# Performance work log

Measured on AMD Instinct MI355X. Metric: run time of the kernel, lower is better.

Reference implementation:

```python
import jax, jax.numpy as jnp
import numpy as np
from jax import lax

NUM_HEADS = 8
FOCUSING_FACTOR = 3.0
KERNEL_SIZE = 5


def setup_inputs() -> dict:
    key = jax.random.key(0)
    ks = jax.random.split(key, 9)
    B, C, H, W = 16, 256, 64, 64
    s = 0.02
    return {
        "x": jax.random.normal(ks[0], (B, C, H, W), dtype=jnp.float32),
        "Wq": jax.random.normal(ks[1], (C, C), dtype=jnp.float32) * s,
        "bq": jax.random.normal(ks[2], (C,), dtype=jnp.float32) * s,
        "Wkv": jax.random.normal(ks[3], (2 * C, C), dtype=jnp.float32) * s,
        "bkv": jax.random.normal(ks[4], (2 * C,), dtype=jnp.float32) * s,
        "Wproj": jax.random.normal(ks[5], (C, C), dtype=jnp.float32) * s,
        "bproj": jax.random.normal(ks[6], (C,), dtype=jnp.float32) * s,
        "dwc_w": jax.random.normal(ks[7], (C // NUM_HEADS, 1, KERNEL_SIZE, KERNEL_SIZE), dtype=jnp.float32) * s,
        "dwc_b": jax.random.normal(ks[8], (C // NUM_HEADS,), dtype=jnp.float32) * s,
        "scale_param": jnp.zeros((1, 1, C), dtype=jnp.float32),
    }


def reference(x, Wq, bq, Wkv, bkv, Wproj, bproj, dwc_w, dwc_b, scale_param):
    B, C, H, W = x.shape
    nh = NUM_HEADS
    hd = C // nh
    N = H * W
    num = int(round(N ** 0.5))  # feature map side, N is a perfect square

    xt = x.reshape(B, C, N).transpose(0, 2, 1)  # [B, N, C]
    q = xt @ Wq.T + bq
    kv = xt @ Wkv.T + bkv  # [B, N, 2C] -> (2, C) split on last dim
    k, v = kv[..., :C], kv[..., C:]
    # positional_encoding is freshly-initialized zeros in the original forward -> no-op

    scale = jax.nn.softplus(scale_param)  # [1, 1, C]
    q = (jax.nn.relu(q) + 1e-6) / scale
    k = (jax.nn.relu(k) + 1e-6) / scale
    q_norm = jnp.linalg.norm(q, axis=-1, keepdims=True)
    k_norm = jnp.linalg.norm(k, axis=-1, keepdims=True)
    q = q ** FOCUSING_FACTOR
    k = k ** FOCUSING_FACTOR
    q = q / jnp.linalg.norm(q, axis=-1, keepdims=True) * q_norm
    k = k / jnp.linalg.norm(k, axis=-1, keepdims=True) * k_norm

    def split_heads(t):  # [B, N, C] -> [B*nh, N, hd]
        return t.reshape(B, N, nh, hd).transpose(0, 2, 1, 3).reshape(B * nh, N, hd)

    q, k, v = split_heads(q), split_heads(k), split_heads(v)

    # linear attention (kv path; i*j*(c+d) > c*d*(i+j) for these shapes)
    z = 1.0 / (jnp.einsum('bic,bc->bi', q, k.sum(axis=1)) + 1e-6)  # [BH, N]
    kv_state = jnp.einsum('bjc,bjd->bcd', k, v)  # [BH, hd, hd]
    out = jnp.einsum('bic,bcd->bid', q, kv_state) * z[..., None]  # [BH, N, hd]

    # depthwise conv on v feature map
    fm = v.transpose(0, 2, 1).reshape(B * nh, hd, num, num)
    fm = lax.conv_general_dilated(
        fm, dwc_w, window_strides=(1, 1),
        padding=[(KERNEL_SIZE // 2, KERNEL_SIZE // 2)] * 2,
        dimension_numbers=('NCHW', 'OIHW', 'NCHW'),
        feature_group_count=hd,
    ) + dwc_b[None, :, None, None]
    fm = fm.reshape(B * nh, hd, N).transpose(0, 2, 1)  # [BH, N, hd]

    out = out + fm
    out = out.reshape(B, nh, N, hd).transpose(0, 2, 1, 3).reshape(B, N, C)
    out = out @ Wproj.T + bproj
    return out.transpose(0, 2, 1).reshape(B, C, H, W)
```

## Files before the change

kernel.cpp:

```cpp
#include <hip/hip_runtime.h>
#include <math.h>

#define NB 16
#define NC 256
#define NN 4096
#define HD 32
#define BHD 128
#define KSPLIT 32

typedef unsigned short bf16_t;
typedef __attribute__((ext_vector_type(4))) float floatx4;
typedef __attribute__((ext_vector_type(16))) float floatx16;
typedef __attribute__((ext_vector_type(8))) short shortx8;

__device__ __forceinline__ float bf2f(unsigned int u16) {
  return __uint_as_float(u16 << 16);
}
__device__ __forceinline__ bf16_t f2bf(float f) {
  unsigned int u = __float_as_uint(f);
  return (bf16_t)((u + 0x7FFFu + ((u >> 16) & 1u)) >> 16);
}
__device__ __forceinline__ void bf8_expand(uint4 u, float* f) {
  f[0] = bf2f(u.x & 0xffffu); f[1] = bf2f(u.x >> 16);
  f[2] = bf2f(u.y & 0xffffu); f[3] = bf2f(u.y >> 16);
  f[4] = bf2f(u.z & 0xffffu); f[5] = bf2f(u.z >> 16);
  f[6] = bf2f(u.w & 0xffffu); f[7] = bf2f(u.w >> 16);
}
__device__ __forceinline__ float softplusf(float x) {
  return fmaxf(x, 0.0f) + log1pf(expf(-fabsf(x)));
}

__device__ __forceinline__ void gl_lds16(const void* g, void* l) {
  __builtin_amdgcn_global_load_lds(
      (const __attribute__((address_space(1))) unsigned int*)g,
      (__attribute__((address_space(3))) unsigned int*)l, 16, 0, 0);
}

__global__ __launch_bounds__(256) void k_prepx(
    const float* __restrict__ x, bf16_t* __restrict__ xbf)
{
  __shared__ float T[64][68];
  const int tid = threadIdx.x;
  const int n0 = blockIdx.x * 64, c0 = blockIdx.y * 64, b = blockIdx.z;
  const float* xb = x + (size_t)b * NC * NN;
#pragma unroll
  for (int it = 0; it < 4; ++it) {
    int c = it * 16 + (tid >> 4);
    int n4 = (tid & 15) * 4;
    float4 v = *(const float4*)(xb + (size_t)(c0 + c) * NN + n0 + n4);
    T[c][n4 + 0] = v.x; T[c][n4 + 1] = v.y;
    T[c][n4 + 2] = v.z; T[c][n4 + 3] = v.w;
  }
  __syncthreads();
  bf16_t* ob = xbf + (size_t)b * NN * NC;
#pragma unroll
  for (int it = 0; it < 2; ++it) {
    int n = it * 32 + (tid >> 3);
    int ch = (tid & 7) * 8;
    unsigned short e[8];
#pragma unroll
    for (int j = 0; j < 8; ++j) e[j] = f2bf(T[ch + j][n]);
    uint4 u;
    u.x = e[0] | ((unsigned)e[1] << 16); u.y = e[2] | ((unsigned)e[3] << 16);
    u.z = e[4] | ((unsigned)e[5] << 16); u.w = e[6] | ((unsigned)e[7] << 16);
    *(uint4*)(ob + (size_t)(n0 + n) * NC + c0 + ch) = u;
  }
}

__global__ __launch_bounds__(256) void k_prepw(
    const float* __restrict__ Wq, const float* __restrict__ Wkv,
    const float* __restrict__ Wp, const float* __restrict__ bq,
    const float* __restrict__ bkv, const float* __restrict__ sp,
    bf16_t* __restrict__ Wqkvb, bf16_t* __restrict__ Wpb,
    float* __restrict__ bias768, float* __restrict__ rscale)
{
  const int blk = blockIdx.x;
  const int tid = threadIdx.x;
  if (blk < 768) {
    const float* src = (blk < 256) ? (Wq + (size_t)blk * NC)
                                   : (Wkv + (size_t)(blk - 256) * NC);
    Wqkvb[(size_t)blk * NC + tid] = f2bf(src[tid]);
  } else if (blk < 1024) {
    int j = blk - 768;
    Wpb[(size_t)j * NC + tid] = f2bf(Wp[(size_t)j * NC + tid]);
  } else if (blk == 1024) {
    for (int i = tid; i < 768; i += 256)
      bias768[i] = (i < 256) ? bq[i] : bkv[i - 256];
  } else {
    rscale[tid] = 1.0f / softplusf(sp[tid]);
  }
}

__global__ __launch_bounds__(256) void k_qkv_mfma(
    const bf16_t* __restrict__ xbf, const bf16_t* __restrict__ Wqkvb,
    const float* __restrict__ bias768, bf16_t* __restrict__ qkv)
{
  __shared__ bf16_t As[128 * 32];
  __shared__ bf16_t Bs[128 * 32];
  const int tid = threadIdx.x;
  const int lane = tid & 63;
  const int w = tid >> 6;
  const int b = blockIdx.z;
  const int m0 = blockIdx.x * 128;
  const int n0 = blockIdx.y * 128;
  const bf16_t* Ab = xbf + ((size_t)b * NN + m0) * NC;
  const bf16_t* Bb = Wqkvb + (size_t)n0 * NC;

  const int wm = (w & 1) * 64;
  const int wn = (w >> 1) * 64;
  const int srow = w * 32 + (lane >> 2);
  const int scol = (((lane & 3) ^ ((lane >> 3) & 3))) * 8;
  const int fm = lane & 15;
  const int kg = lane >> 4;
  const int kga = kg ^ ((fm >> 1) & 3);

  floatx4 acc[4][4];
#pragma unroll
  for (int i = 0; i < 4; ++i)
#pragma unroll
    for (int j = 0; j < 4; ++j) {
      floatx4 z = {0.f, 0.f, 0.f, 0.f};
      acc[i][j] = z;
    }

  for (int k0 = 0; k0 < NC; k0 += 32) {
#pragma unroll
    for (int r = 0; r < 2; ++r) {
      gl_lds16(Ab + (size_t)(srow + r * 16) * NC + k0 + scol,
               &As[(w * 32 + r * 16) * 32]);
      gl_lds16(Bb + (size_t)(srow + r * 16) * NC + k0 + scol,
               &Bs[(w * 32 + r * 16) * 32]);
    }
    __syncthreads();
    shortx8 af[4], bfg[4];
#pragma unroll
    for (int t = 0; t < 4; ++t) {
      af[t]  = *(const shortx8*)&As[(wm + t * 16 + fm) * 32 + kga * 8];
      bfg[t] = *(const shortx8*)&Bs[(wn + t * 16 + fm) * 32 + kga * 8];
    }
#pragma unroll
    for (int tm = 0; tm < 4; ++tm)
#pragma unroll
      for (int tn = 0; tn < 4; ++tn)
        acc[tm][tn] = __builtin_amdgcn_mfma_f32_16x16x32_bf16(
            af[tm], bfg[tn], acc[tm][tn], 0, 0, 0);
    __syncthreads();
  }

  float bv[4];
#pragma unroll
  for (int tn = 0; tn < 4; ++tn)
    bv[tn] = bias768[n0 + wn + tn * 16 + fm];

  bf16_t* obase = qkv + ((size_t)b * NN + m0) * 768;
#pragma unroll
  for (int tm = 0; tm < 4; ++tm) {
    int mrow = wm + tm * 16 + kg * 4;
#pragma unroll
    for (int tn = 0; tn < 4; ++tn) {
      int n = n0 + wn + tn * 16 + fm;
#pragma unroll
      for (int r = 0; r < 4; ++r)
        obase[(size_t)(mrow + r) * 768 + n] = f2bf(acc[tm][tn][r] + bv[tn]);
    }
  }
}

__global__ __launch_bounds__(256) void k_focus(
    bf16_t* __restrict__ qkv, const float* __restrict__ rscale)
{
  const int lane = threadIdx.x & 63;
  const int w = threadIdx.x >> 6;
  const size_t t = (size_t)blockIdx.x * 4 + w;
  bf16_t* row = qkv + t * 768;
  ushort4 qu = *(ushort4*)(row + lane * 4);
  ushort4 ku = *(ushort4*)(row + 256 + lane * 4);
  float4 s4 = *(const float4*)(rscale + lane * 4);
  float q[4] = {bf2f(qu.x), bf2f(qu.y), bf2f(qu.z), bf2f(qu.w)};
  float k[4] = {bf2f(ku.x), bf2f(ku.y), bf2f(ku.z), bf2f(ku.w)};
  float rs[4] = {s4.x, s4.y, s4.z, s4.w};
  float q3[4], k3[4];
  float sq2 = 0.f, sq6 = 0.f, sk2 = 0.f, sk6 = 0.f;
#pragma unroll
  for (int i = 0; i < 4; ++i) {
    float qi = (fmaxf(q[i], 0.f) + 1e-6f) * rs[i];
    float ki = (fmaxf(k[i], 0.f) + 1e-6f) * rs[i];
    float qc = qi * qi * qi;
    float kc = ki * ki * ki;
    sq2 += qi * qi;  sk2 += ki * ki;
    sq6 += qc * qc;  sk6 += kc * kc;
    q3[i] = qc; k3[i] = kc;
  }
#pragma unroll
  for (int off = 32; off > 0; off >>= 1) {
    sq2 += __shfl_xor(sq2, off);
    sq6 += __shfl_xor(sq6, off);
    sk2 += __shfl_xor(sk2, off);
    sk6 += __shfl_xor(sk6, off);
  }
  float qs = sqrtf(sq2) * rsqrtf(sq6);
  float ks = sqrtf(sk2) * rsqrtf(sk6);
  ushort4 qo, ko;
  qo.x = f2bf(q3[0] * qs); qo.y = f2bf(q3[1] * qs);
  qo.z = f2bf(q3[2] * qs); qo.w = f2bf(q3[3] * qs);
  ko.x = f2bf(k3[0] * ks); ko.y = f2bf(k3[1] * ks);
  ko.z = f2bf(k3[2] * ks); ko.w = f2bf(k3[3] * ks);
  *(ushort4*)(row + lane * 4) = qo;
  *(ushort4*)(row + 256 + lane * 4) = ko;
}

__global__ __launch_bounds__(256) void k_kvstate(
    const bf16_t* __restrict__ qkv, float* __restrict__ kvsp,
    float* __restrict__ ksump)
{
  const int tid = threadIdx.x;
  const int lane = tid & 63;
  const int w = tid >> 6;
  const int bh = blockIdx.x;
  const int spl = blockIdx.y * 4 + w;
  const int b = bh >> 3, h = bh & 7;
  const int c = lane & 31;
  const int g = lane >> 5;

  floatx16 acc;
#pragma unroll
  for (int r = 0; r < 16; ++r) acc[r] = 0.f;
  float ksacc = 0.f;

  const bf16_t* kp = qkv + ((size_t)b * NN + (size_t)spl * (NN / KSPLIT) + g * 8) * 768
                     + 256 + h * HD + c;
#pragma unroll 2
  for (int s = 0; s < (NN / KSPLIT) / 16; ++s) {
    unsigned short av[8], bv[8];
#pragma unroll
    for (int e = 0; e < 8; ++e) {
      av[e] = kp[(size_t)e * 768];
      bv[e] = kp[(size_t)e * 768 + 256];
    }
    shortx8 af, bfg;
#pragma unroll
    for (int e = 0; e < 8; ++e) {
      af[e] = (short)av[e];
      bfg[e] = (short)bv[e];
      ksacc += bf2f(av[e]);
    }
    acc = __builtin_amdgcn_mfma_f32_32x32x16_bf16(af, bfg, acc, 0, 0, 0);
    kp += 16 * 768;
  }

  float* op = kvsp + ((size_t)spl * BHD + bh) * (HD * HD);
#pragma unroll
  for (int r = 0; r < 16; ++r) {
    int row = (r & 3) + 8 * (r >> 2) + 4 * g;
    op[row * HD + c] = acc[r];
  }
  ksacc += __shfl_xor(ksacc, 32);
  if (g == 0) ksump[((size_t)spl * BHD + bh) * HD + c] = ksacc;
}

__global__ __launch_bounds__(256) void k_combine(
    const float* __restrict__ kvsp, const float* __restrict__ ksump,
    bf16_t* __restrict__ kvTb, bf16_t* __restrict__ ksumb)
{
  const int gid = blockIdx.x * 256 + threadIdx.x;
  const int bh = gid >> 10;
  const int cd = gid & 1023;
  const int cc = cd >> 5, d = cd & 31;
  float v = 0.f;
  const float* p = kvsp + (size_t)bh * (HD * HD) + cd;
#pragma unroll
  for (int s = 0; s < KSPLIT; ++s) v += p[(size_t)s * BHD * (HD * HD)];
  kvTb[(size_t)bh * (HD * HD) + d * HD + cc] = f2bf(v);
  if (cd < HD) {
    float u = 0.f;
    const float* q = ksump + (size_t)bh * HD + cd;
#pragma unroll
    for (int s = 0; s < KSPLIT; ++s) u += q[(size_t)s * BHD * HD];
    ksumb[(size_t)bh * HD + cd] = f2bf(u);
  }
}

#define VT_STRIDE 548
__global__ __launch_bounds__(256) void k_attnout(
    const bf16_t* __restrict__ qkv, const bf16_t* __restrict__ kvTb,
    const bf16_t* __restrict__ ksumb, const float* __restrict__ dwc_w,
    const float* __restrict__ dwc_b, bf16_t* __restrict__ attn)
{
  __shared__ bf16_t vt[32 * VT_STRIDE];
  __shared__ bf16_t mvz[256 * 32];
  const int tid = threadIdx.x;
  const int lane = tid & 63;
  const int w = tid >> 6;
  const int s = blockIdx.x;
  const int bh = blockIdx.y;
  const int b = bh >> 3, h = bh & 7;

#pragma unroll
  for (int it = 0; it < 8; ++it) {
    int idx = it * 256 + tid;
    int ry = idx >> 8;
    int col = (idx >> 2) & 63;
    int slot = idx & 3;
    int y = s * 4 - 2 + ry;
    uint4 u = make_uint4(0u, 0u, 0u, 0u);
    if (y >= 0 && y < 64)
      u = *(const uint4*)(qkv + ((size_t)b * NN + y * 64 + col) * 768 + 512 + h * HD + slot * 8);
    unsigned short e[8];
    e[0] = (unsigned short)(u.x & 0xffffu); e[1] = (unsigned short)(u.x >> 16);
    e[2] = (unsigned short)(u.y & 0xffffu); e[3] = (unsigned short)(u.y >> 16);
    e[4] = (unsigned short)(u.z & 0xffffu); e[5] = (unsigned short)(u.z >> 16);
    e[6] = (unsigned short)(u.w & 0xffffu); e[7] = (unsigned short)(u.w >> 16);
#pragma unroll
    for (int j = 0; j < 8; ++j)
      vt[(slot * 8 + j) * VT_STRIDE + (col + 2) * 8 + ry] = e[j];
  }
#pragma unroll
  for (int e = 0; e < 4; ++e) {
    int idx = tid * 4 + e;
    int d = idx >> 5;
    int rem = idx & 31;
    int cc4 = rem >> 3;
    int ry = rem & 7;
    int cc = (cc4 < 2) ? cc4 : (64 + cc4);
    vt[d * VT_STRIDE + cc * 8 + ry] = 0;
  }

  const int fm = lane & 15;
  const int kg = lane >> 4;
  shortx8 b0 = *(const shortx8*)(kvTb + (size_t)bh * 1024 + fm * HD + kg * 8);
  shortx8 b1 = *(const shortx8*)(kvTb + (size_t)bh * 1024 + (16 + fm) * HD + kg * 8);
  shortx8 b2 = {0, 0, 0, 0, 0, 0, 0, 0};
  if (fm == 0) b2 = *(const shortx8*)(ksumb + (size_t)bh * HD + kg * 8);
  floatx4 zf = {0.f, 0.f, 0.f, 0.f};
#pragma unroll
  for (int q = 0; q < 4; ++q) {
    int mt = w * 4 + q;
    int tok = s * 256 + mt * 16 + fm;
    shortx8 a = *(const shortx8*)(qkv + ((size_t)b * NN + tok) * 768 + h * HD + kg * 8);
    floatx4 d0 = __builtin_amdgcn_mfma_f32_16x16x32_bf16(a, b0, zf, 0, 0, 0);
    floatx4 d1 = __builtin_amdgcn_mfma_f32_16x16x32_bf16(a, b1, zf, 0, 0, 0);
    floatx4 d2 = __builtin_amdgcn_mfma_f32_16x16x32_bf16(a, b2, zf, 0, 0, 0);
#pragma unroll
    for (int r = 0; r < 4; ++r) {
      float qk = __shfl(d2[r], lane & 48);
      float z = 1.0f / (qk + 1e-6f);
      int tl = mt * 16 + kg * 4 + r;
      mvz[tl * 32 + fm] = f2bf(d0[r] * z);
      mvz[tl * 32 + 16 + fm] = f2bf(d1[r] * z);
    }
  }
  __syncthreads();

  const int d = tid & 31;
  const int xg = tid >> 5;
  const int x0c = xg * 8;
  float wr[25];
#pragma unroll
  for (int j = 0; j < 25; ++j) wr[j] = dwc_w[d * 25 + j];
  const float bd = dwc_b[d];
  const bf16_t* vd = vt + d * VT_STRIDE;

  float win[5][8];
#define LOADCOL(dst, cc) do {                                   \
    const bf16_t* _p = vd + (cc) * 8;                           \
    uint2 _u0 = *(const uint2*)_p;                              \
    uint2 _u1 = *(const uint2*)(_p + 4);                        \
    (dst)[0] = bf2f(_u0.x & 0xffffu); (dst)[1] = bf2f(_u0.x >> 16); \
    (dst)[2] = bf2f(_u0.y & 0xffffu); (dst)[3] = bf2f(_u0.y >> 16); \
    (dst)[4] = bf2f(_u1.x & 0xffffu); (dst)[5] = bf2f(_u1.x >> 16); \
    (dst)[6] = bf2f(_u1.y & 0xffffu); (dst)[7] = bf2f(_u1.y >> 16); \
  } while (0)

#pragma unroll
  for (int p = 0; p < 4; ++p) LOADCOL(win[p], x0c + p);

  bf16_t* arow = attn + ((size_t)b * NN + s * 256) * NC + h * HD + d;
#pragma unroll
  for (int i = 0; i < 8; ++i) {
    int x = x0c + i;
    LOADCOL(win[4], x + 4);
#pragma unroll
    for (int ty = 0; ty < 4; ++ty) {
      float acc = bd;
#pragma unroll
      for (int ky = 0; ky < 5; ++ky)
#pragma unroll
        for (int kx = 0; kx < 5; ++kx)
          acc += wr[ky * 5 + kx] * win[kx][ty + ky];
      int tl = ty * 64 + x;
      acc += bf2f(mvz[tl * 32 + d]);
      arow[(size_t)tl * NC] = f2bf(acc);
    }
#pragma unroll
    for (int c2 = 0; c2 < 4; ++c2)
#pragma unroll
      for (int r2 = 0; r2 < 8; ++r2) win[c2][r2] = win[c2 + 1][r2];
  }
#undef LOADCOL
}

__global__ __launch_bounds__(256) void k_proj_mfma(
    const bf16_t* __restrict__ attn, const bf16_t* __restrict__ Wpb,
    const float* __restrict__ bp, float* __restrict__ out)
{
  __shared__ bf16_t As[128 * 32];
  __shared__ bf16_t Bs[128 * 32];
  const int tid = threadIdx.x;
  const int lane = tid & 63;
  const int w = tid >> 6;
  const size_t m0 = (size_t)blockIdx.x * 128;
  const int n0 = blockIdx.y * 128;
  const bf16_t* Ab = attn + m0 * NC;
  const bf16_t* Bb = Wpb + (size_t)n0 * NC;

  const int wm = (w & 1) * 64;
  const int wn = (w >> 1) * 64;
  const int srow = w * 32 + (lane >> 2);
  const int scol = (((lane & 3) ^ ((lane >> 3) & 3))) * 8;
  const int fm = lane & 15;
  const int kg = lane >> 4;
  const int kga = kg ^ ((fm >> 1) & 3);

  floatx4 acc[4][4];
#pragma unroll
  for (int i = 0; i < 4; ++i)
#pragma unroll
    for (int j = 0; j < 4; ++j) {
      floatx4 z = {0.f, 0.f, 0.f, 0.f};
      acc[i][j] = z;
    }

  for (int k0 = 0; k0 < NC; k0 += 32) {
#pragma unroll
    for (int r = 0; r < 2; ++r) {
      gl_lds16(Ab + (size_t)(srow + r * 16) * NC + k0 + scol,
               &As[(w * 32 + r * 16) * 32]);
      gl_lds16(Bb + (size_t)(srow + r * 16) * NC + k0 + scol,
               &Bs[(w * 32 + r * 16) * 32]);
    }
    __syncthreads();
    shortx8 af[4], bfg[4];
#pragma unroll
    for (int t = 0; t < 4; ++t) {
      af[t]  = *(const shortx8*)&As[(wm + t * 16 + fm) * 32 + kga * 8];
      bfg[t] = *(const shortx8*)&Bs[(wn + t * 16 + fm) * 32 + kga * 8];
    }
#pragma unroll
    for (int tm = 0; tm < 4; ++tm)
#pragma unroll
      for (int tn = 0; tn < 4; ++tn)
        acc[tm][tn] = __builtin_amdgcn_mfma_f32_16x16x32_bf16(
            af[tm], bfg[tn], acc[tm][tn], 0, 0, 0);
    __syncthreads();
  }

  const int b = (int)(m0 >> 12);
  const int t0 = (int)(m0 & 4095);
  float* ob = out + (size_t)b * NC * NN;
#pragma unroll
  for (int tn = 0; tn < 4; ++tn) {
    int j = n0 + wn + tn * 16 + fm;
    float bj = bp[j];
#pragma unroll
    for (int tm = 0; tm < 4; ++tm) {
      int trow = t0 + wm + tm * 16 + kg * 4;
      float4 o;
      o.x = acc[tm][tn][0] + bj;
      o.y = acc[tm][tn][1] + bj;
      o.z = acc[tm][tn][2] + bj;
      o.w = acc[tm][tn][3] + bj;
      *(float4*)(ob + (size_t)j * NN + trow) = o;
    }
  }
}

extern "C" void kernel_launch(void* const* d_in, const int* in_sizes, int n_in,
                              void* d_out, int out_size, void* d_ws, size_t ws_size,
                              hipStream_t stream)
{
  (void)in_sizes; (void)n_in; (void)out_size; (void)ws_size;
  const float* x    = (const float*)d_in[0];
  const float* Wq   = (const float*)d_in[1];
  const float* bq   = (const float*)d_in[2];
  const float* Wkv  = (const float*)d_in[3];
  const float* bkv  = (const float*)d_in[4];
  const float* Wp   = (const float*)d_in[5];
  const float* bp   = (const float*)d_in[6];
  const float* dwcw = (const float*)d_in[7];
  const float* dwcb = (const float*)d_in[8];
  const float* sp   = (const float*)d_in[9];
  float* out = (float*)d_out;

  char* wsb = (char*)d_ws;
  bf16_t* qkv  = (bf16_t*)wsb;
  bf16_t* attn = (bf16_t*)(wsb + 100663296u);
  bf16_t* xbf  = attn;
  float*  kvsp  = (float*)attn;
  float*  ksump = (float*)(wsb + 100663296u + 16777216u);
  char*   tail  = wsb + 100663296u + 33554432u + 2097152u + 65536u;
  bf16_t* kvTb  = (bf16_t*)tail;
  bf16_t* ksumb = kvTb + (size_t)BHD * HD * HD;
  bf16_t* Wqkvb = ksumb + (size_t)BHD * HD;
  bf16_t* Wpb   = Wqkvb + 768 * 256;
  float*  bias768 = (float*)(Wpb + 256 * 256);
  float*  rscale  = bias768 + 768;

  k_prepx<<<dim3(64, 4, 16), 256, 0, stream>>>(x, xbf);
  k_prepw<<<1026, 256, 0, stream>>>(Wq, Wkv, Wp, bq, bkv, sp, Wqkvb, Wpb, bias768, rscale);
  k_qkv_mfma<<<dim3(32, 6, 16), 256, 0, stream>>>(xbf, Wqkvb, bias768, qkv);
  k_focus<<<16384, 256, 0, stream>>>(qkv, rscale);
  k_kvstate<<<dim3(BHD, KSPLIT / 4), 256, 0, stream>>>(qkv, kvsp, ksump);
  k_combine<<<512, 256, 0, stream>>>(kvsp, ksump, kvTb, ksumb);
  k_attnout<<<dim3(16, BHD), 256, 0, stream>>>(qkv, kvTb, ksumb, dwcw, dwcb, attn);
  k_proj_mfma<<<dim3(512, 2), 256, 0, stream>>>(attn, Wpb, bp, out);
}
```

Before: 286.9 us.

## Fuse focusing normalization into QKV GEMM epilogue with full-row N tiles

The QKV GEMM tile becomes 64 tokens by 256 channels, so each block holds complete q, k or v rows. The relu, scale, cube and norm-ratio focusing step then runs in the epilogue, using shuffle and LDS reductions across the four waves. This removes the separate k_focus kernel and its extra read and write pass over the q/k buffer. In exchange the tile shape is less square, so the A tile gets less reuse, and the epilogue adds synchronizations and register pressure.

```diff
diff --git a/kernel.cpp b/kernel.cpp
--- a/kernel.cpp
+++ b/kernel.cpp
@@ -19,12 +19,6 @@
 __device__ __forceinline__ bf16_t f2bf(float f) {
   unsigned int u = __float_as_uint(f);
   return (bf16_t)((u + 0x7FFFu + ((u >> 16) & 1u)) >> 16);
-}
-__device__ __forceinline__ void bf8_expand(uint4 u, float* f) {
-  f[0] = bf2f(u.x & 0xffffu); f[1] = bf2f(u.x >> 16);
-  f[2] = bf2f(u.y & 0xffffu); f[3] = bf2f(u.y >> 16);
-  f[4] = bf2f(u.z & 0xffffu); f[5] = bf2f(u.z >> 16);
-  f[6] = bf2f(u.w & 0xffffu); f[7] = bf2f(u.w >> 16);
 }
 __device__ __forceinline__ float softplusf(float x) {
   return fmaxf(x, 0.0f) + log1pf(expf(-fabsf(x)));
@@ -93,22 +87,26 @@
 
 __global__ __launch_bounds__(256) void k_qkv_mfma(
     const bf16_t* __restrict__ xbf, const bf16_t* __restrict__ Wqkvb,
-    const float* __restrict__ bias768, bf16_t* __restrict__ qkv)
-{
-  __shared__ bf16_t As[128 * 32];
-  __shared__ bf16_t Bs[128 * 32];
+    const float* __restrict__ bias768, const float* __restrict__ rscale,
+    bf16_t* __restrict__ qkv)
+{
+  __shared__ bf16_t As[64 * 32];
+  __shared__ bf16_t Bs[256 * 32];
+  __shared__ float red2[4][64];
+  __shared__ float red6[4][64];
+  __shared__ float qsf[64];
   const int tid = threadIdx.x;
   const int lane = tid & 63;
   const int w = tid >> 6;
   const int b = blockIdx.z;
-  const int m0 = blockIdx.x * 128;
-  const int n0 = blockIdx.y * 128;
+  const int m0 = blockIdx.x * 64;
+  const int n0b = blockIdx.y;
   const bf16_t* Ab = xbf + ((size_t)b * NN + m0) * NC;
-  const bf16_t* Bb = Wqkvb + (size_t)n0 * NC;
-
-  const int wm = (w & 1) * 64;
-  const int wn = (w >> 1) * 64;
-  const int srow = w * 32 + (lane >> 2);
+  const bf16_t* Bb = Wqkvb + (size_t)n0b * 256 * NC;
+
+  const int wn = w * 64;
+  const int arow = w * 16 + (lane >> 2);
+  const int brow = w * 64 + (lane >> 2);
   const int scol = (((lane & 3) ^ ((lane >> 3) & 3))) * 8;
   const int fm = lane & 15;
   const int kg = lane >> 4;
@@ -124,18 +122,16 @@
     }
 
   for (int k0 = 0; k0 < NC; k0 += 32) {
-#pragma unroll
-    for (int r = 0; r < 2; ++r) {
-      gl_lds16(Ab + (size_t)(srow + r * 16) * NC + k0 + scol,
-               &As[(w * 32 + r * 16) * 32]);
-      gl_lds16(Bb + (size_t)(srow + r * 16) * NC + k0 + scol,
-               &Bs[(w * 32 + r * 16) * 32]);
-    }
+    gl_lds16(Ab + (size_t)arow * NC + k0 + scol, &As[(w * 16) * 32]);
+#pragma unroll
+    for (int r = 0; r < 4; ++r)
+      gl_lds16(Bb + (size_t)(brow + r * 16) * NC + k0 + scol,
+               &Bs[(w * 64 + r * 16) * 32]);
     __syncthreads();
     shortx8 af[4], bfg[4];
 #pragma unroll
     for (int t = 0; t < 4; ++t) {
-      af[t]  = *(const shortx8*)&As[(wm + t * 16 + fm) * 32 + kga * 8];
+      af[t]  = *(const shortx8*)&As[(t * 16 + fm) * 32 + kga * 8];
       bfg[t] = *(const shortx8*)&Bs[(wn + t * 16 + fm) * 32 + kga * 8];
     }
 #pragma unroll
@@ -147,66 +143,87 @@
     __syncthreads();
   }
 
-  float bv[4];
-#pragma unroll
-  for (int tn = 0; tn < 4; ++tn)
-    bv[tn] = bias768[n0 + wn + tn * 16 + fm];
-
-  bf16_t* obase = qkv + ((size_t)b * NN + m0) * 768;
-#pragma unroll
-  for (int tm = 0; tm < 4; ++tm) {
-    int mrow = wm + tm * 16 + kg * 4;
+  bf16_t* obase = qkv + ((size_t)b * NN + m0) * 768 + n0b * 256;
+
+  if (n0b == 2) {
+    float bv[4];
+#pragma unroll
+    for (int tn = 0; tn < 4; ++tn)
+      bv[tn] = bias768[512 + wn + tn * 16 + fm];
+#pragma unroll
+    for (int tm = 0; tm < 4; ++tm)
+#pragma unroll
+      for (int tn = 0; tn < 4; ++tn)
+#pragma unroll
+        for (int r = 0; r < 4; ++r) {
+          int tl = tm * 16 + kg * 4 + r;
+          obase[(size_t)tl * 768 + wn + tn * 16 + fm] =
+              f2bf(acc[tm][tn][r] + bv[tn]);
+        }
+  } else {
+    float bv[4], rsv[4];
 #pragma unroll
     for (int tn = 0; tn < 4; ++tn) {
-      int n = n0 + wn + tn * 16 + fm;
-#pragma unroll
-      for (int r = 0; r < 4; ++r)
-        obase[(size_t)(mrow + r) * 768 + n] = f2bf(acc[tm][tn][r] + bv[tn]);
-    }
-  }
-}
-
-__global__ __launch_bounds__(256) void k_focus(
-    bf16_t* __restrict__ qkv, const float* __restrict__ rscale)
-{
-  const int lane = threadIdx.x & 63;
-  const int w = threadIdx.x >> 6;
-  const size_t t = (size_t)blockIdx.x * 4 + w;
-  bf16_t* row = qkv + t * 768;
-  ushort4 qu = *(ushort4*)(row + lane * 4);
-  ushort4 ku = *(ushort4*)(row + 256 + lane * 4);
-  float4 s4 = *(const float4*)(rscale + lane * 4);
-  float q[4] = {bf2f(qu.x), bf2f(qu.y), bf2f(qu.z), bf2f(qu.w)};
-  float k[4] = {bf2f(ku.x), bf2f(ku.y), bf2f(ku.z), bf2f(ku.w)};
-  float rs[4] = {s4.x, s4.y, s4.z, s4.w};
-  float q3[4], k3[4];
-  float sq2 = 0.f, sq6 = 0.f, sk2 = 0.f, sk6 = 0.f;
-#pragma unroll
-  for (int i = 0; i < 4; ++i) {
-    float qi = (fmaxf(q[i], 0.f) + 1e-6f) * rs[i];
-    float ki = (fmaxf(k[i], 0.f) + 1e-6f) * rs[i];
-    float qc = qi * qi * qi;
-    float kc = ki * ki * ki;
-    sq2 += qi * qi;  sk2 += ki * ki;
-    sq6 += qc * qc;  sk6 += kc * kc;
-    q3[i] = qc; k3[i] = kc;
-  }
-#pragma unroll
-  for (int off = 32; off > 0; off >>= 1) {
-    sq2 += __shfl_xor(sq2, off);
-    sq6 += __shfl_xor(sq6, off);
-    sk2 += __shfl_xor(sk2, off);
-    sk6 += __shfl_xor(sk6, off);
-  }
-  float qs = sqrtf(sq2) * rsqrtf(sq6);
-  float ks = sqrtf(sk2) * rsqrtf(sk6);
-  ushort4 qo, ko;
-  qo.x = f2bf(q3[0] * qs); qo.y = f2bf(q3[1] * qs);
-  qo.z = f2bf(q3[2] * qs); qo.w = f2bf(q3[3] * qs);
-  ko.x = f2bf(k3[0] * ks); ko.y = f2bf(k3[1] * ks);
-  ko.z = f2bf(k3[2] * ks); ko.w = f2bf(k3[3] * ks);
-  *(ushort4*)(row + lane * 4) = qo;
-  *(ushort4*)(row + 256 + lane * 4) = ko;
+      int ch = wn + tn * 16 + fm;
+      bv[tn] = bias768[n0b * 256 + ch];
+      rsv[tn] = rscale[ch];
+    }
+    float s2[4][4], s6[4][4];
+#pragma unroll
+    for (int tm = 0; tm < 4; ++tm)
+#pragma unroll
+      for (int r = 0; r < 4; ++r) { s2[tm][r] = 0.f; s6[tm][r] = 0.f; }
+#pragma unroll
+    for (int tm = 0; tm < 4; ++tm)
+#pragma unroll
+      for (int tn = 0; tn < 4; ++tn)
+#pragma unroll
+        for (int r = 0; r < 4; ++r) {
+          float qi = (fmaxf(acc[tm][tn][r] + bv[tn], 0.f) + 1e-6f) * rsv[tn];
+          float q3 = qi * qi * qi;
+          acc[tm][tn][r] = q3;
+          s2[tm][r] += qi * qi;
+          s6[tm][r] += q3 * q3;
+        }
+#pragma unroll
+    for (int off = 1; off < 16; off <<= 1)
+#pragma unroll
+      for (int tm = 0; tm < 4; ++tm)
+#pragma unroll
+        for (int r = 0; r < 4; ++r) {
+          s2[tm][r] += __shfl_xor(s2[tm][r], off);
+          s6[tm][r] += __shfl_xor(s6[tm][r], off);
+        }
+    if (fm == 0) {
+#pragma unroll
+      for (int tm = 0; tm < 4; ++tm)
+#pragma unroll
+        for (int r = 0; r < 4; ++r) {
+          int tl = tm * 16 + kg * 4 + r;
+          red2[w][tl] = s2[tm][r];
+          red6[w][tl] = s6[tm][r];
+        }
+    }
+    __syncthreads();
+    if (tid < 64) {
+      float S2 = 0.f, S6 = 0.f;
+#pragma unroll
+      for (int w4 = 0; w4 < 4; ++w4) { S2 += red2[w4][tid]; S6 += red6[w4][tid]; }
+      qsf[tid] = sqrtf(S2) * rsqrtf(S6);
+    }
+    __syncthreads();
+#pragma unroll
+    for (int tm = 0; tm < 4; ++tm)
+#pragma unroll
+      for (int r = 0; r < 4; ++r) {
+        int tl = tm * 16 + kg * 4 + r;
+        float qs = qsf[tl];
+#pragma unroll
+        for (int tn = 0; tn < 4; ++tn)
+          obase[(size_t)tl * 768 + wn + tn * 16 + fm] =
+              f2bf(acc[tm][tn][r] * qs);
+      }
+  }
 }
 
 __global__ __launch_bounds__(256) void k_kvstate(
@@ -507,8 +524,7 @@
 
   k_prepx<<<dim3(64, 4, 16), 256, 0, stream>>>(x, xbf);
   k_prepw<<<1026, 256, 0, stream>>>(Wq, Wkv, Wp, bq, bkv, sp, Wqkvb, Wpb, bias768, rscale);
-  k_qkv_mfma<<<dim3(32, 6, 16), 256, 0, stream>>>(xbf, Wqkvb, bias768, qkv);
-  k_focus<<<16384, 256, 0, stream>>>(qkv, rscale);
+  k_qkv_mfma<<<dim3(64, 3, 16), 256, 0, stream>>>(xbf, Wqkvb, bias768, rscale, qkv);
   k_kvstate<<<dim3(BHD, KSPLIT / 4), 256, 0, stream>>>(qkv, kvsp, ksump);
   k_combine<<<512, 256, 0, stream>>>(kvsp, ksump, kvTb, ksumb);
   k_attnout<<<dim3(16, BHD), 256, 0, stream>>>(qkv, kvTb, ksumb, dwcw, dwcb, attn);
```

Measured after the change: 308.7 us. 7.6% more time.
